# Kernel optimization log

Measured on AMD Instinct MI355X. Metric: run time of the kernel, lower is better.

## Reference

```python
import jax, jax.numpy as jnp
import numpy as np

B, D_MODEL, N, H = 4, 256, 2048, 4
DIM = D_MODEL // H  # 64


def setup_inputs() -> dict:
    k = jax.random.key(0)
    ks = jax.random.split(k, 11)
    mk = lambda kk, shape, s=1.0: jax.random.normal(kk, shape, dtype=jnp.float32) * s
    return {
        'query': mk(ks[0], (B, D_MODEL, N)),
        'key': mk(ks[1], (B, D_MODEL, N)),
        'value': mk(ks[2], (B, D_MODEL, N)),
        # 1x1 Conv1d == per-position linear: weight [out, in], bias [out]
        'wq': mk(ks[3], (D_MODEL, D_MODEL), 0.05), 'bq': mk(ks[4], (D_MODEL,), 0.05),
        'wk': mk(ks[5], (D_MODEL, D_MODEL), 0.05), 'bk': mk(ks[6], (D_MODEL,), 0.05),
        'wv': mk(ks[7], (D_MODEL, D_MODEL), 0.05), 'bv': mk(ks[8], (D_MODEL,), 0.05),
        'wm': mk(ks[9], (D_MODEL, D_MODEL), 0.05), 'bm': mk(ks[10], (D_MODEL,), 0.05),
    }


def _proj(x, w, b):
    # Conv1d(kernel_size=1): [b, c_in, n] -> [b, c_out, n]
    return jnp.einsum('oc,bcn->bon', w, x) + b[None, :, None]


def reference(query, key, value, wq, bq, wk, bk, wv, bv, wm, bm):
    b = query.shape[0]
    # project and split channels d_model -> (dim, h); matches torch .view(b, dim, h, -1)
    q = _proj(query, wq, bq).reshape(b, DIM, H, -1)
    kk = _proj(key, wk, bk).reshape(b, DIM, H, -1)
    v = _proj(value, wv, bv).reshape(b, DIM, H, -1)
    scores = jnp.einsum('bdhn,bdhm->bhnm', q, kk) / jnp.sqrt(jnp.float32(DIM))
    prob = jax.nn.softmax(scores, axis=-1)  # [b, h, n, m]
    x = jnp.einsum('bhnm,bdhm->bdhn', prob, v)
    return _proj(x.reshape(b, DIM * H, -1), wm, bm)
```

## Files before the change

### kernel.cpp

```cpp
#include <hip/hip_runtime.h>
#include <hip/hip_bf16.h>

#define DMODEL 256
#define NSEQ   2048
#define NB     4
#define NH     4
#define DHEAD  64

typedef __attribute__((ext_vector_type(8))) short short8;
typedef __attribute__((ext_vector_type(4))) float float4v;
typedef __attribute__((ext_vector_type(2))) float float2v;
typedef __attribute__((ext_vector_type(2))) unsigned int uint2v;
typedef unsigned short u16;

#define AS1 __attribute__((address_space(1)))
#define AS3 __attribute__((address_space(3)))

static __device__ inline u16 f2bf(float f) {
    unsigned u = __builtin_bit_cast(unsigned, f);
    u += 0x7fffu + ((u >> 16) & 1u);
    return (u16)(u >> 16);
}
static __device__ inline unsigned pk2(float a, float b) {
    __hip_bfloat162 h = __float22bfloat162_rn(make_float2(a, b));
    unsigned r;
    __builtin_memcpy(&r, &h, 4);
    return r;
}
static __device__ inline float max3f(float a, float b, float c) {
    return fmaxf(fmaxf(a, b), c);
}
static __device__ inline float tmax16(const float4v* s) {
    float a = max3f(s[0][0], s[0][1], s[0][2]);
    float b = max3f(s[0][3], s[1][0], s[1][1]);
    float c = max3f(s[1][2], s[1][3], s[2][0]);
    float d = max3f(s[2][1], s[2][2], s[2][3]);
    float e = max3f(s[3][0], s[3][1], s[3][2]);
    float f = max3f(a, b, c);
    float g = max3f(d, e, s[3][3]);
    return fmaxf(f, g);
}

__global__ __launch_bounds__(256) void convert_x_kernel(
    const float* __restrict__ xq, const float* __restrict__ xk,
    const float* __restrict__ xv, u16* __restrict__ xt_ws)
{
    const int nt = blockIdx.x;
    const int ct = blockIdx.y;
    const int z  = blockIdx.z;
    const int b = z / 3, mode = z % 3;
    const float* X = ((mode == 0) ? xq : (mode == 1) ? xk : xv) + (size_t)b * DMODEL * NSEQ;
    u16* dst = xt_ws + (size_t)z * NSEQ * DMODEL;

    __shared__ u16 t[64][72];
    const int tid = threadIdx.x;

    #pragma unroll
    for (int i = 0; i < 4; i++) {
        int e = tid + i * 256;
        int c = e >> 4;
        int n4 = (e & 15) * 4;
        float4v v = *(const float4v*)&X[(size_t)(ct * 64 + c) * NSEQ + nt * 64 + n4];
        #pragma unroll
        for (int j = 0; j < 4; j++) {
            int row = n4 + j;
            int fr = (row & 7) ^ ((row >> 3) & 7);
            t[row][(((c >> 3) ^ fr) << 3) + (c & 7)] = f2bf(v[j]);
        }
    }
    __syncthreads();
    #pragma unroll
    for (int i = 0; i < 4; i++) {
        int e = tid + i * 256;
        int n = e >> 4;
        int cb = (e & 15) * 4;
        int fr = (n & 7) ^ ((n >> 3) & 7);
        uint2v val = *(const uint2v*)&t[n][(((cb >> 3) ^ fr) << 3) + (cb & 7)];
        *(uint2v*)&dst[(size_t)(nt * 64 + n) * DMODEL + ct * 64 + cb] = val;
    }
}

__global__ __launch_bounds__(256) void wpack_kernel(
    const float* __restrict__ wq, const float* __restrict__ wk,
    const float* __restrict__ wv, const float* __restrict__ wm,
    u16* __restrict__ wbf)
{
    const int sr = blockIdx.x, m = blockIdx.y, tcol = threadIdx.x;
    const float* W = (m == 0) ? wq : (m == 1) ? wk : (m == 2) ? wv : wm;
    float v;
    if (m < 3) {
        int og = (sr & ~15) | ((sr & 3) << 2) | ((sr >> 2) & 3);
        v = W[(size_t)og * DMODEL + tcol];
    } else {
        int c = ((tcol & 63) << 2) | (tcol >> 6);
        v = W[(size_t)sr * DMODEL + c];
    }
    wbf[(size_t)m * 65536 + (size_t)sr * DMODEL + tcol] = f2bf(v);
}

__global__ __launch_bounds__(256) void proj_qkv_kernel(
    const u16* __restrict__ xt_ws, const u16* __restrict__ wbf,
    const float* __restrict__ bqp, const float* __restrict__ bkp, const float* __restrict__ bvp,
    u16* __restrict__ q_ws, u16* __restrict__ k_ws, u16* __restrict__ vt_ws)
{
    const int nt0 = blockIdx.x, ot = blockIdx.y, bz = blockIdx.z;
    const int b = bz / 3, mode = bz % 3;
    const float* BI = (mode == 0) ? bqp : (mode == 1) ? bkp : bvp;

    const int tid = threadIdx.x;
    const int wave = tid >> 6, lane = tid & 63;
    const int g = lane >> 4, ql = lane & 15;
    const int srow8 = lane >> 3, su = lane & 7;
    const int u_l = su ^ srow8;
    const int obase = ot * 64, nbase = nt0 * 64;

    const u16* Asrc = wbf + (size_t)mode * 65536;
    const u16* Bsrc = xt_ws + (size_t)bz * (NSEQ * DMODEL);

    __shared__ u16 at[2][64][64];
    __shared__ u16 bt[2][64][64];

    float4v acc[4];
    #pragma unroll
    for (int i = 0; i < 4; i++) acc[i] = (float4v){0.f, 0.f, 0.f, 0.f};

    #define PSTAGE(bufi_, c0_)                                                         \
        { _Pragma("unroll")                                                            \
          for (int p_ = 0; p_ < 2; p_++) {                                             \
            int rb_ = wave * 8 + p_ * 32;                                              \
            int row_ = rb_ + srow8;                                                    \
            __builtin_amdgcn_global_load_lds(                                          \
                (const AS1 unsigned int*)(Asrc + (size_t)(obase + row_) * DMODEL + (c0_) + u_l * 8), \
                (AS3 unsigned int*)&at[bufi_][rb_][0], 16, 0, 0);                      \
            __builtin_amdgcn_global_load_lds(                                          \
                (const AS1 unsigned int*)(Bsrc + (size_t)(nbase + row_) * DMODEL + (c0_) + u_l * 8), \
                (AS3 unsigned int*)&bt[bufi_][rb_][0], 16, 0, 0);                      \
          } }

    PSTAGE(0, 0)
    __syncthreads();
    int buf = 0;
    const int sw = ql & 7;
    #pragma unroll
    for (int t = 0; t < 4; t++) {
        if (t < 3) PSTAGE(buf ^ 1, (t + 1) * 64)
        #pragma unroll
        for (int kc = 0; kc < 2; kc++) {
            short8 afrag = *(const short8*)&at[buf][wave * 16 + ql][(((kc * 4 + g) ^ sw)) * 8];
            #pragma unroll
            for (int nt = 0; nt < 4; nt++) {
                short8 bfrag = *(const short8*)&bt[buf][nt * 16 + ql][(((kc * 4 + g) ^ sw)) * 8];
                acc[nt] = __builtin_amdgcn_mfma_f32_16x16x32_bf16(afrag, bfrag, acc[nt], 0, 0, 0);
            }
        }
        __syncthreads();
        buf ^= 1;
    }
    #undef PSTAGE

    const int h = g;
    const int d0 = (obase + wave * 16) >> 2;
    float bias[4];
    #pragma unroll
    for (int r = 0; r < 4; r++) bias[r] = BI[obase + wave * 16 + 4 * r + g];

    #pragma unroll
    for (int nt = 0; nt < 4; nt++) {
        int n = nbase + nt * 16 + ql;
        float v[4];
        #pragma unroll
        for (int r = 0; r < 4; r++) v[r] = acc[nt][r] + bias[r];
        if (mode == 0) {
            #pragma unroll
            for (int r = 0; r < 4; r++) v[r] *= 0.18033688011112042f;
            uint2v pk = {pk2(v[0], v[1]), pk2(v[2], v[3])};
            *(uint2v*)&q_ws[((size_t)(b * NH + h) * NSEQ + n) * DHEAD + d0] = pk;
        } else if (mode == 1) {
            uint2v pk = {pk2(v[0], v[1]), pk2(v[2], v[3])};
            *(uint2v*)&k_ws[((size_t)(b * NH + h) * NSEQ + n) * DHEAD + d0] = pk;
        } else {
            #pragma unroll
            for (int r = 0; r < 4; r++)
                vt_ws[((size_t)(b * NH + h) * DHEAD + d0 + r) * NSEQ + n] = f2bf(v[r]);
        }
    }
}

__global__ __launch_bounds__(256) void attn_kernel(
    const u16* __restrict__ q_ws, const u16* __restrict__ k_ws,
    const u16* __restrict__ vt_ws, u16* __restrict__ x_hs)
{
    const int bid = blockIdx.x;
    const int orig = (bid & 7) * 32 + (bid >> 3);
    const int bh = orig >> 4;
    const int qt128 = orig & 15;
    const int tid = threadIdx.x;
    const int wave = tid >> 6, lane = tid & 63;
    const int g = lane >> 4, ql = lane & 15;
    const int qbase = qt128 * 128 + wave * 32;

    const u16* qp = q_ws + ((size_t)bh * NSEQ + qbase) * DHEAD;
    const u16* kp = k_ws + (size_t)bh * NSEQ * DHEAD;
    const u16* vp = vt_ws + (size_t)bh * DHEAD * NSEQ;

    __shared__ u16 kt[2][64][64];
    __shared__ u16 vt[2][64][64];
    __shared__ u16 p_lds[4][2][16][72];

    const int srow = lane >> 3;
    const int su_l = lane & 7;
    const int u_l  = su_l ^ srow;
    const int swz  = ql & 7;

    short8 qf[2][2];
    #pragma unroll
    for (int qt = 0; qt < 2; qt++)
        #pragma unroll
        for (int kc = 0; kc < 2; kc++)
            qf[qt][kc] = *(const short8*)(qp + (size_t)(qt * 16 + ql) * DHEAD + kc * 32 + g * 8);

    float4v acc[2][4];
    #pragma unroll
    for (int qt = 0; qt < 2; qt++)
        #pragma unroll
        for (int t = 0; t < 4; t++) acc[qt][t] = (float4v){0.f, 0.f, 0.f, 0.f};
    float m0 = -INFINITY, m1 = -INFINITY, l0 = 0.f, l1 = 0.f;

    #define STAGE(mb_, bufi_)                                                          \
        {                                                                              \
            _Pragma("unroll")                                                          \
            for (int i_ = 0; i_ < 2; i_++) {                                           \
                int row_ = wave * 16 + i_ * 8 + srow;                                  \
                __builtin_amdgcn_global_load_lds(                                      \
                    (const AS1 unsigned int*)(kp + (size_t)((mb_) + row_) * DHEAD + u_l * 8), \
                    (AS3 unsigned int*)&kt[bufi_][wave * 16 + i_ * 8][0], 16, 0, 0);   \
                __builtin_amdgcn_global_load_lds(                                      \
                    (const AS1 unsigned int*)(vp + (size_t)row_ * NSEQ + (mb_) + u_l * 8), \
                    (AS3 unsigned int*)&vt[bufi_][wave * 16 + i_ * 8][0], 16, 0, 0);   \
            }                                                                          \
        }

    STAGE(0, 0);
    __syncthreads();

    int buf = 0;
    for (int t = 0; t < NSEQ / 64; t++) {
        const int mb = t * 64;
        if (t < NSEQ / 64 - 1) STAGE(mb + 64, buf ^ 1);

        float4v st[2][4];
        #pragma unroll
        for (int qt = 0; qt < 2; qt++)
            #pragma unroll
            for (int mt = 0; mt < 4; mt++) st[qt][mt] = (float4v){0.f, 0.f, 0.f, 0.f};
        #pragma unroll
        for (int mt = 0; mt < 4; mt++) {
            #pragma unroll
            for (int kc = 0; kc < 2; kc++) {
                short8 kf = *(const short8*)&kt[buf][mt * 16 + ql][((kc * 4 + g) ^ swz) * 8];
                st[0][mt] = __builtin_amdgcn_mfma_f32_16x16x32_bf16(kf, qf[0][kc], st[0][mt], 0, 0, 0);
                st[1][mt] = __builtin_amdgcn_mfma_f32_16x16x32_bf16(kf, qf[1][kc], st[1][mt], 0, 0, 0);
            }
        }

        float tmax0 = tmax16(&st[0][0]);
        float tmax1 = tmax16(&st[1][0]);
        tmax0 = fmaxf(tmax0, __shfl_xor(tmax0, 16, 64));
        tmax0 = fmaxf(tmax0, __shfl_xor(tmax0, 32, 64));
        tmax1 = fmaxf(tmax1, __shfl_xor(tmax1, 16, 64));
        tmax1 = fmaxf(tmax1, __shfl_xor(tmax1, 32, 64));

        bool need = (tmax0 > m0 + 8.f) || (tmax1 > m1 + 8.f);
        if (__any(need)) {
            float mn0 = fmaxf(m0, tmax0), mn1 = fmaxf(m1, tmax1);
            float a0 = __builtin_amdgcn_exp2f(m0 - mn0);
            float a1 = __builtin_amdgcn_exp2f(m1 - mn1);
            #pragma unroll
            for (int tt = 0; tt < 4; tt++)
                #pragma unroll
                for (int r = 0; r < 4; r++) {
                    acc[0][tt][r] *= a0;
                    acc[1][tt][r] *= a1;
                }
            l0 *= a0; l1 *= a1;
            m0 = mn0; m1 = mn1;
        }

        float2v s0v = {0.f, 0.f}, s1v = {0.f, 0.f};
        #pragma unroll
        for (int mt = 0; mt < 4; mt++) {
            float p00 = __builtin_amdgcn_exp2f(st[0][mt][0] - m0);
            float p01 = __builtin_amdgcn_exp2f(st[0][mt][1] - m0);
            float p02 = __builtin_amdgcn_exp2f(st[0][mt][2] - m0);
            float p03 = __builtin_amdgcn_exp2f(st[0][mt][3] - m0);
            s0v += (float2v){p00, p01};
            s0v += (float2v){p02, p03};
            *(uint2v*)&p_lds[wave][0][ql][mt * 16 + g * 4] = (uint2v){pk2(p00, p01), pk2(p02, p03)};
            float p10 = __builtin_amdgcn_exp2f(st[1][mt][0] - m1);
            float p11 = __builtin_amdgcn_exp2f(st[1][mt][1] - m1);
            float p12 = __builtin_amdgcn_exp2f(st[1][mt][2] - m1);
            float p13 = __builtin_amdgcn_exp2f(st[1][mt][3] - m1);
            s1v += (float2v){p10, p11};
            s1v += (float2v){p12, p13};
            *(uint2v*)&p_lds[wave][1][ql][mt * 16 + g * 4] = (uint2v){pk2(p10, p11), pk2(p12, p13)};
        }
        float ps0 = s0v[0] + s0v[1], ps1 = s1v[0] + s1v[1];
        ps0 += __shfl_xor(ps0, 16, 64);
        ps0 += __shfl_xor(ps0, 32, 64);
        ps1 += __shfl_xor(ps1, 16, 64);
        ps1 += __shfl_xor(ps1, 32, 64);
        l0 += ps0; l1 += ps1;

        #pragma unroll
        for (int kc = 0; kc < 2; kc++) {
            short8 pf0 = *(const short8*)&p_lds[wave][0][ql][kc * 32 + g * 8];
            short8 pf1 = *(const short8*)&p_lds[wave][1][ql][kc * 32 + g * 8];
            #pragma unroll
            for (int tt = 0; tt < 4; tt++) {
                short8 vf = *(const short8*)&vt[buf][tt * 16 + ql][((kc * 4 + g) ^ swz) * 8];
                acc[0][tt] = __builtin_amdgcn_mfma_f32_16x16x32_bf16(vf, pf0, acc[0][tt], 0, 0, 0);
                acc[1][tt] = __builtin_amdgcn_mfma_f32_16x16x32_bf16(vf, pf1, acc[1][tt], 0, 0, 0);
            }
        }
        __syncthreads();
        buf ^= 1;
    }
    #undef STAGE

    float inv0 = 1.f / l0, inv1 = 1.f / l1;
    #pragma unroll
    for (int qt = 0; qt < 2; qt++) {
        float inv = qt ? inv1 : inv0;
        u16* xrow = x_hs + ((size_t)bh * NSEQ + qbase + qt * 16 + ql) * DHEAD;
        #pragma unroll
        for (int t = 0; t < 4; t++) {
            uint2v pk = {pk2(acc[qt][t][0] * inv, acc[qt][t][1] * inv),
                         pk2(acc[qt][t][2] * inv, acc[qt][t][3] * inv)};
            *(uint2v*)&xrow[t * 16 + g * 4] = pk;
        }
    }
}

__global__ __launch_bounds__(256) void proj_out_kernel(
    const u16* __restrict__ x_hs, const u16* __restrict__ wbf,
    const float* __restrict__ bm, float* __restrict__ out)
{
    const int nt0 = blockIdx.x, ot = blockIdx.y, b = blockIdx.z;

    const int tid = threadIdx.x;
    const int wave = tid >> 6, lane = tid & 63;
    const int g = lane >> 4, ql = lane & 15;
    const int srow8 = lane >> 3, su = lane & 7;
    const int u_l = su ^ srow8;
    const int obase = ot * 64, nbase = nt0 * 64;

    const u16* Asrc = wbf + (size_t)3 * 65536;

    __shared__ u16 at[2][64][64];
    __shared__ u16 bt[2][64][64];

    float4v acc[4];
    #pragma unroll
    for (int i = 0; i < 4; i++) acc[i] = (float4v){0.f, 0.f, 0.f, 0.f};

    #define OSTAGE(bufi_, c0_)                                                         \
        { _Pragma("unroll")                                                            \
          for (int p_ = 0; p_ < 2; p_++) {                                             \
            int rb_ = wave * 8 + p_ * 32;                                              \
            int row_ = rb_ + srow8;                                                    \
            __builtin_amdgcn_global_load_lds(                                          \
                (const AS1 unsigned int*)(Asrc + (size_t)(obase + row_) * DMODEL + (c0_) + u_l * 8), \
                (AS3 unsigned int*)&at[bufi_][rb_][0], 16, 0, 0);                      \
            __builtin_amdgcn_global_load_lds(                                          \
                (const AS1 unsigned int*)(x_hs + ((size_t)(b * NH + ((c0_) >> 6)) * NSEQ + nbase + row_) * DHEAD + u_l * 8), \
                (AS3 unsigned int*)&bt[bufi_][rb_][0], 16, 0, 0);                      \
          } }

    OSTAGE(0, 0)
    __syncthreads();
    int buf = 0;
    const int sw = ql & 7;
    #pragma unroll
    for (int t = 0; t < 4; t++) {
        if (t < 3) OSTAGE(buf ^ 1, (t + 1) * 64)
        #pragma unroll
        for (int kc = 0; kc < 2; kc++) {
            short8 afrag = *(const short8*)&at[buf][wave * 16 + ql][(((kc * 4 + g) ^ sw)) * 8];
            #pragma unroll
            for (int nt = 0; nt < 4; nt++) {
                short8 bfrag = *(const short8*)&bt[buf][nt * 16 + ql][(((kc * 4 + g) ^ sw)) * 8];
                acc[nt] = __builtin_amdgcn_mfma_f32_16x16x32_bf16(afrag, bfrag, acc[nt], 0, 0, 0);
            }
        }
        __syncthreads();
        buf ^= 1;
    }
    #undef OSTAGE

    const int o0 = obase + wave * 16 + g * 4;
    #pragma unroll
    for (int nt = 0; nt < 4; nt++) {
        int n = nbase + nt * 16 + ql;
        #pragma unroll
        for (int r = 0; r < 4; r++) {
            int o = o0 + r;
            out[((size_t)b * DMODEL + o) * NSEQ + n] = acc[nt][r] + bm[o];
        }
    }
}

extern "C" void kernel_launch(void* const* d_in, const int* in_sizes, int n_in,
                              void* d_out, int out_size, void* d_ws, size_t ws_size,
                              hipStream_t stream)
{
    const float* query = (const float*)d_in[0];
    const float* key   = (const float*)d_in[1];
    const float* value = (const float*)d_in[2];
    const float* wq = (const float*)d_in[3];
    const float* bq = (const float*)d_in[4];
    const float* wk = (const float*)d_in[5];
    const float* bk = (const float*)d_in[6];
    const float* wv = (const float*)d_in[7];
    const float* bv = (const float*)d_in[8];
    const float* wm = (const float*)d_in[9];
    const float* bm = (const float*)d_in[10];
    float* out = (float*)d_out;

    char* ws = (char*)d_ws;
    const size_t SEG = (size_t)NB * NH * NSEQ * DHEAD * sizeof(u16);
    u16* q_ws  = (u16*)(ws);
    u16* k_ws  = (u16*)(ws + SEG);
    u16* vt_ws = (u16*)(ws + 2 * SEG);
    u16* x_hs  = (u16*)(ws + 3 * SEG);
    u16* xt_ws = (u16*)(ws + 4 * SEG);
    u16* wbf   = (u16*)(ws + 4 * SEG + (size_t)12 * NSEQ * DMODEL * sizeof(u16));

    convert_x_kernel<<<dim3(32, 4, 12), 256, 0, stream>>>(query, key, value, xt_ws);
    wpack_kernel<<<dim3(256, 4), 256, 0, stream>>>(wq, wk, wv, wm, wbf);
    proj_qkv_kernel<<<dim3(32, 4, 12), 256, 0, stream>>>(
        xt_ws, wbf, bq, bk, bv, q_ws, k_ws, vt_ws);
    attn_kernel<<<dim3(256), 256, 0, stream>>>(q_ws, k_ws, vt_ws, x_hs);
    proj_out_kernel<<<dim3(32, 4, NB), 256, 0, stream>>>(x_hs, wbf, bm, out);
}
```

Before: 162.5 us.

## Use 8 waves per attention block and merge prep kernels

The attention kernel now runs 512 threads per block, so each wave handles 16 query rows instead of 32 and each wave stages half as much K/V per tile. This doubles the number of waves sharing each K/V tile and cuts per-wave register use, aiming for better latency hiding. The x-transpose and weight-pack kernels are merged into one launch to save a launch. The bf16 pack helper is replaced with a manual round-to-nearest bit routine. In exchange, each K tile load now serves fewer query rows per wave, and more waves wait at every block barrier.

```diff
diff --git a/kernel.cpp b/kernel.cpp
--- a/kernel.cpp
+++ b/kernel.cpp
@@ -9,7 +9,6 @@
 
 typedef __attribute__((ext_vector_type(8))) short short8;
 typedef __attribute__((ext_vector_type(4))) float float4v;
-typedef __attribute__((ext_vector_type(2))) float float2v;
 typedef __attribute__((ext_vector_type(2))) unsigned int uint2v;
 typedef unsigned short u16;
 
@@ -21,11 +20,8 @@
     u += 0x7fffu + ((u >> 16) & 1u);
     return (u16)(u >> 16);
 }
-static __device__ inline unsigned pk2(float a, float b) {
-    __hip_bfloat162 h = __float22bfloat162_rn(make_float2(a, b));
-    unsigned r;
-    __builtin_memcpy(&r, &h, 4);
-    return r;
+static __device__ inline unsigned pack2bf(float a, float b) {
+    return (unsigned)f2bf(a) | ((unsigned)f2bf(b) << 16);
 }
 static __device__ inline float max3f(float a, float b, float c) {
     return fmaxf(fmaxf(a, b), c);
@@ -41,19 +37,40 @@
     return fmaxf(f, g);
 }
 
-__global__ __launch_bounds__(256) void convert_x_kernel(
+__global__ __launch_bounds__(256) void prep_kernel(
     const float* __restrict__ xq, const float* __restrict__ xk,
-    const float* __restrict__ xv, u16* __restrict__ xt_ws)
+    const float* __restrict__ xv,
+    const float* __restrict__ wq, const float* __restrict__ wk,
+    const float* __restrict__ wv, const float* __restrict__ wm,
+    u16* __restrict__ xt_ws, u16* __restrict__ wbf)
 {
-    const int nt = blockIdx.x;
-    const int ct = blockIdx.y;
-    const int z  = blockIdx.z;
+    const int bid = blockIdx.x;
+    const int tid = threadIdx.x;
+
+    if (bid >= 1536) {
+        const int id = bid - 1536;
+        const int sr = id & 255, m = id >> 8;
+        const float* W = (m == 0) ? wq : (m == 1) ? wk : (m == 2) ? wv : wm;
+        float v;
+        if (m < 3) {
+            int og = (sr & ~15) | ((sr & 3) << 2) | ((sr >> 2) & 3);
+            v = W[(size_t)og * DMODEL + tid];
+        } else {
+            int c = ((tid & 63) << 2) | (tid >> 6);
+            v = W[(size_t)sr * DMODEL + c];
+        }
+        wbf[(size_t)m * 65536 + (size_t)sr * DMODEL + tid] = f2bf(v);
+        return;
+    }
+
+    const int nt = bid & 31;
+    const int ct = (bid >> 5) & 3;
+    const int z  = bid >> 7;
     const int b = z / 3, mode = z % 3;
     const float* X = ((mode == 0) ? xq : (mode == 1) ? xk : xv) + (size_t)b * DMODEL * NSEQ;
     u16* dst = xt_ws + (size_t)z * NSEQ * DMODEL;
 
     __shared__ u16 t[64][72];
-    const int tid = threadIdx.x;
 
     #pragma unroll
     for (int i = 0; i < 4; i++) {
@@ -78,24 +95,6 @@
         uint2v val = *(const uint2v*)&t[n][(((cb >> 3) ^ fr) << 3) + (cb & 7)];
         *(uint2v*)&dst[(size_t)(nt * 64 + n) * DMODEL + ct * 64 + cb] = val;
     }
-}
-
-__global__ __launch_bounds__(256) void wpack_kernel(
-    const float* __restrict__ wq, const float* __restrict__ wk,
-    const float* __restrict__ wv, const float* __restrict__ wm,
-    u16* __restrict__ wbf)
-{
-    const int sr = blockIdx.x, m = blockIdx.y, tcol = threadIdx.x;
-    const float* W = (m == 0) ? wq : (m == 1) ? wk : (m == 2) ? wv : wm;
-    float v;
-    if (m < 3) {
-        int og = (sr & ~15) | ((sr & 3) << 2) | ((sr >> 2) & 3);
-        v = W[(size_t)og * DMODEL + tcol];
-    } else {
-        int c = ((tcol & 63) << 2) | (tcol >> 6);
-        v = W[(size_t)sr * DMODEL + c];
-    }
-    wbf[(size_t)m * 65536 + (size_t)sr * DMODEL + tcol] = f2bf(v);
 }
 
 __global__ __launch_bounds__(256) void proj_qkv_kernel(
@@ -173,10 +172,10 @@
         if (mode == 0) {
             #pragma unroll
             for (int r = 0; r < 4; r++) v[r] *= 0.18033688011112042f;
-            uint2v pk = {pk2(v[0], v[1]), pk2(v[2], v[3])};
+            uint2v pk = {pack2bf(v[0], v[1]), pack2bf(v[2], v[3])};
             *(uint2v*)&q_ws[((size_t)(b * NH + h) * NSEQ + n) * DHEAD + d0] = pk;
         } else if (mode == 1) {
-            uint2v pk = {pk2(v[0], v[1]), pk2(v[2], v[3])};
+            uint2v pk = {pack2bf(v[0], v[1]), pack2bf(v[2], v[3])};
             *(uint2v*)&k_ws[((size_t)(b * NH + h) * NSEQ + n) * DHEAD + d0] = pk;
         } else {
             #pragma unroll
@@ -186,7 +185,7 @@
     }
 }
 
-__global__ __launch_bounds__(256) void attn_kernel(
+__global__ __launch_bounds__(512) void attn_kernel(
     const u16* __restrict__ q_ws, const u16* __restrict__ k_ws,
     const u16* __restrict__ vt_ws, u16* __restrict__ x_hs)
 {
@@ -197,7 +196,7 @@
     const int tid = threadIdx.x;
     const int wave = tid >> 6, lane = tid & 63;
     const int g = lane >> 4, ql = lane & 15;
-    const int qbase = qt128 * 128 + wave * 32;
+    const int qbase = qt128 * 128 + wave * 16;
 
     const u16* qp = q_ws + ((size_t)bh * NSEQ + qbase) * DHEAD;
     const u16* kp = k_ws + (size_t)bh * NSEQ * DHEAD;
@@ -205,39 +204,32 @@
 
     __shared__ u16 kt[2][64][64];
     __shared__ u16 vt[2][64][64];
-    __shared__ u16 p_lds[4][2][16][72];
+    __shared__ u16 p_lds[8][16][72];
 
     const int srow = lane >> 3;
     const int su_l = lane & 7;
     const int u_l  = su_l ^ srow;
     const int swz  = ql & 7;
 
-    short8 qf[2][2];
-    #pragma unroll
-    for (int qt = 0; qt < 2; qt++)
-        #pragma unroll
-        for (int kc = 0; kc < 2; kc++)
-            qf[qt][kc] = *(const short8*)(qp + (size_t)(qt * 16 + ql) * DHEAD + kc * 32 + g * 8);
-
-    float4v acc[2][4];
-    #pragma unroll
-    for (int qt = 0; qt < 2; qt++)
-        #pragma unroll
-        for (int t = 0; t < 4; t++) acc[qt][t] = (float4v){0.f, 0.f, 0.f, 0.f};
-    float m0 = -INFINITY, m1 = -INFINITY, l0 = 0.f, l1 = 0.f;
+    short8 qf[2];
+    #pragma unroll
+    for (int kc = 0; kc < 2; kc++)
+        qf[kc] = *(const short8*)(qp + (size_t)ql * DHEAD + kc * 32 + g * 8);
+
+    float4v acc[4];
+    #pragma unroll
+    for (int t = 0; t < 4; t++) acc[t] = (float4v){0.f, 0.f, 0.f, 0.f};
+    float mrun = -INFINITY, lrun = 0.f;
 
     #define STAGE(mb_, bufi_)                                                          \
         {                                                                              \
-            _Pragma("unroll")                                                          \
-            for (int i_ = 0; i_ < 2; i_++) {                                           \
-                int row_ = wave * 16 + i_ * 8 + srow;                                  \
-                __builtin_amdgcn_global_load_lds(                                      \
-                    (const AS1 unsigned int*)(kp + (size_t)((mb_) + row_) * DHEAD + u_l * 8), \
-                    (AS3 unsigned int*)&kt[bufi_][wave * 16 + i_ * 8][0], 16, 0, 0);   \
-                __builtin_amdgcn_global_load_lds(                                      \
-                    (const AS1 unsigned int*)(vp + (size_t)row_ * NSEQ + (mb_) + u_l * 8), \
-                    (AS3 unsigned int*)&vt[bufi_][wave * 16 + i_ * 8][0], 16, 0, 0);   \
-            }                                                                          \
+            int row_ = wave * 8 + srow;                                                \
+            __builtin_amdgcn_global_load_lds(                                          \
+                (const AS1 unsigned int*)(kp + (size_t)((mb_) + row_) * DHEAD + u_l * 8), \
+                (AS3 unsigned int*)&kt[bufi_][wave * 8][0], 16, 0, 0);                 \
+            __builtin_amdgcn_global_load_lds(                                          \
+                (const AS1 unsigned int*)(vp + (size_t)row_ * NSEQ + (mb_) + u_l * 8), \
+                (AS3 unsigned int*)&vt[bufi_][wave * 8][0], 16, 0, 0);                 \
         }
 
     STAGE(0, 0);
@@ -248,78 +240,54 @@
         const int mb = t * 64;
         if (t < NSEQ / 64 - 1) STAGE(mb + 64, buf ^ 1);
 
-        float4v st[2][4];
-        #pragma unroll
-        for (int qt = 0; qt < 2; qt++)
-            #pragma unroll
-            for (int mt = 0; mt < 4; mt++) st[qt][mt] = (float4v){0.f, 0.f, 0.f, 0.f};
+        float4v st[4];
+        #pragma unroll
+        for (int mt = 0; mt < 4; mt++) st[mt] = (float4v){0.f, 0.f, 0.f, 0.f};
         #pragma unroll
         for (int mt = 0; mt < 4; mt++) {
             #pragma unroll
             for (int kc = 0; kc < 2; kc++) {
                 short8 kf = *(const short8*)&kt[buf][mt * 16 + ql][((kc * 4 + g) ^ swz) * 8];
-                st[0][mt] = __builtin_amdgcn_mfma_f32_16x16x32_bf16(kf, qf[0][kc], st[0][mt], 0, 0, 0);
-                st[1][mt] = __builtin_amdgcn_mfma_f32_16x16x32_bf16(kf, qf[1][kc], st[1][mt], 0, 0, 0);
+                st[mt] = __builtin_amdgcn_mfma_f32_16x16x32_bf16(kf, qf[kc], st[mt], 0, 0, 0);
             }
         }
 
-        float tmax0 = tmax16(&st[0][0]);
-        float tmax1 = tmax16(&st[1][0]);
-        tmax0 = fmaxf(tmax0, __shfl_xor(tmax0, 16, 64));
-        tmax0 = fmaxf(tmax0, __shfl_xor(tmax0, 32, 64));
-        tmax1 = fmaxf(tmax1, __shfl_xor(tmax1, 16, 64));
-        tmax1 = fmaxf(tmax1, __shfl_xor(tmax1, 32, 64));
-
-        bool need = (tmax0 > m0 + 8.f) || (tmax1 > m1 + 8.f);
-        if (__any(need)) {
-            float mn0 = fmaxf(m0, tmax0), mn1 = fmaxf(m1, tmax1);
-            float a0 = __builtin_amdgcn_exp2f(m0 - mn0);
-            float a1 = __builtin_amdgcn_exp2f(m1 - mn1);
+        float tmax = tmax16(&st[0]);
+        tmax = fmaxf(tmax, __shfl_xor(tmax, 16, 64));
+        tmax = fmaxf(tmax, __shfl_xor(tmax, 32, 64));
+
+        if (__any(tmax > mrun + 8.f)) {
+            float mnew = fmaxf(mrun, tmax);
+            float a = __builtin_amdgcn_exp2f(mrun - mnew);
             #pragma unroll
             for (int tt = 0; tt < 4; tt++)
                 #pragma unroll
-                for (int r = 0; r < 4; r++) {
-                    acc[0][tt][r] *= a0;
-                    acc[1][tt][r] *= a1;
-                }
-            l0 *= a0; l1 *= a1;
-            m0 = mn0; m1 = mn1;
-        }
-
-        float2v s0v = {0.f, 0.f}, s1v = {0.f, 0.f};
+                for (int r = 0; r < 4; r++) acc[tt][r] *= a;
+            lrun *= a;
+            mrun = mnew;
+        }
+
+        float psum = 0.f;
         #pragma unroll
         for (int mt = 0; mt < 4; mt++) {
-            float p00 = __builtin_amdgcn_exp2f(st[0][mt][0] - m0);
-            float p01 = __builtin_amdgcn_exp2f(st[0][mt][1] - m0);
-            float p02 = __builtin_amdgcn_exp2f(st[0][mt][2] - m0);
-            float p03 = __builtin_amdgcn_exp2f(st[0][mt][3] - m0);
-            s0v += (float2v){p00, p01};
-            s0v += (float2v){p02, p03};
-            *(uint2v*)&p_lds[wave][0][ql][mt * 16 + g * 4] = (uint2v){pk2(p00, p01), pk2(p02, p03)};
-            float p10 = __builtin_amdgcn_exp2f(st[1][mt][0] - m1);
-            float p11 = __builtin_amdgcn_exp2f(st[1][mt][1] - m1);
-            float p12 = __builtin_amdgcn_exp2f(st[1][mt][2] - m1);
-            float p13 = __builtin_amdgcn_exp2f(st[1][mt][3] - m1);
-            s1v += (float2v){p10, p11};
-            s1v += (float2v){p12, p13};
-            *(uint2v*)&p_lds[wave][1][ql][mt * 16 + g * 4] = (uint2v){pk2(p10, p11), pk2(p12, p13)};
-        }
-        float ps0 = s0v[0] + s0v[1], ps1 = s1v[0] + s1v[1];
-        ps0 += __shfl_xor(ps0, 16, 64);
-        ps0 += __shfl_xor(ps0, 32, 64);
-        ps1 += __shfl_xor(ps1, 16, 64);
-        ps1 += __shfl_xor(ps1, 32, 64);
-        l0 += ps0; l1 += ps1;
+            float p0 = __builtin_amdgcn_exp2f(st[mt][0] - mrun);
+            float p1 = __builtin_amdgcn_exp2f(st[mt][1] - mrun);
+            float p2 = __builtin_amdgcn_exp2f(st[mt][2] - mrun);
+            float p3 = __builtin_amdgcn_exp2f(st[mt][3] - mrun);
+            psum += (p0 + p1) + (p2 + p3);
+            *(uint2v*)&p_lds[wave][ql][mt * 16 + g * 4] = (uint2v){pack2bf(p0, p1), pack2bf(p2, p3)};
+        }
+        psum += __shfl_xor(psum, 16, 64);
+        psum += __shfl_xor(psum, 32, 64);
+        lrun += psum;
 
         #pragma unroll
         for (int kc = 0; kc < 2; kc++) {
-            short8 pf0 = *(const short8*)&p_lds[wave][0][ql][kc * 32 + g * 8];
-            short8 pf1 = *(const short8*)&p_lds[wave][1][ql][kc * 32 + g * 8];
+            short8 pf = *(const short8*)&p_lds[wave][ql][kc * 32 + g * 8];
             #pragma unroll
             for (int tt = 0; tt < 4; tt++) {
                 short8 vf = *(const short8*)&vt[buf][tt * 16 + ql][((kc * 4 + g) ^ swz) * 8];
-                acc[0][tt] = __builtin_amdgcn_mfma_f32_16x16x32_bf16(vf, pf0, acc[0][tt], 0, 0, 0);
-                acc[1][tt] = __builtin_amdgcn_mfma_f32_16x16x32_bf16(vf, pf1, acc[1][tt], 0, 0, 0);
+                acc[tt] = __builtin_amdgcn_mfma_f32_16x16x32_bf16(vf, pf, acc[tt], 0, 0, 0);
             }
         }
         __syncthreads();
@@ -327,17 +295,13 @@
     }
     #undef STAGE
 
-    float inv0 = 1.f / l0, inv1 = 1.f / l1;
-    #pragma unroll
-    for (int qt = 0; qt < 2; qt++) {
-        float inv = qt ? inv1 : inv0;
-        u16* xrow = x_hs + ((size_t)bh * NSEQ + qbase + qt * 16 + ql) * DHEAD;
-        #pragma unroll
-        for (int t = 0; t < 4; t++) {
-            uint2v pk = {pk2(acc[qt][t][0] * inv, acc[qt][t][1] * inv),
-                         pk2(acc[qt][t][2] * inv, acc[qt][t][3] * inv)};
-            *(uint2v*)&xrow[t * 16 + g * 4] = pk;
-        }
+    float inv = 1.f / lrun;
+    u16* xrow = x_hs + ((size_t)bh * NSEQ + qbase + ql) * DHEAD;
+    #pragma unroll
+    for (int t = 0; t < 4; t++) {
+        uint2v pk = {pack2bf(acc[t][0] * inv, acc[t][1] * inv),
+                     pack2bf(acc[t][2] * inv, acc[t][3] * inv)};
+        *(uint2v*)&xrow[t * 16 + g * 4] = pk;
     }
 }
 
@@ -435,10 +399,10 @@
     u16* xt_ws = (u16*)(ws + 4 * SEG);
     u16* wbf   = (u16*)(ws + 4 * SEG + (size_t)12 * NSEQ * DMODEL * sizeof(u16));
 
-    convert_x_kernel<<<dim3(32, 4, 12), 256, 0, stream>>>(query, key, value, xt_ws);
-    wpack_kernel<<<dim3(256, 4), 256, 0, stream>>>(wq, wk, wv, wm, wbf);
+    prep_kernel<<<dim3(2560), 256, 0, stream>>>(
+        query, key, value, wq, wk, wv, wm, xt_ws, wbf);
     proj_qkv_kernel<<<dim3(32, 4, 12), 256, 0, stream>>>(
         xt_ws, wbf, bq, bk, bv, q_ws, k_ws, vt_ws);
-    attn_kernel<<<dim3(256), 256, 0, stream>>>(q_ws, k_ws, vt_ws, x_hs);
+    attn_kernel<<<dim3(256), 512, 0, stream>>>(q_ws, k_ws, vt_ws, x_hs);
     proj_out_kernel<<<dim3(32, 4, NB), 256, 0, stream>>>(x_hs, wbf, bm, out);
 }
```

Result: faster. 155.3 us (-4.5%).
